# Kernel optimization log

Measured on AMD Instinct MI355X. Metric: run time of the kernel, lower is better.

The kernel has to match this reference:

```python
import jax, jax.numpy as jnp
import numpy as np

# Product-key memory config (matches init_kwargs)
HEADS = 4
K_DIM = 512          # per-head query/key dim; split in two halves of 256
HALF = K_DIM // 2
V_DIM = 512
SUBSIZE = 512        # sub-keys per bank; value table size = SUBSIZE**2
SIZE = SUBSIZE * SUBSIZE
TOPK = 8
TEMP = 1.0
B, T = 4, 2048


def setup_inputs() -> dict:
    key = jax.random.key(0)
    kq, kk, kv = jax.random.split(key, 3)
    bound = 1.0 / np.sqrt(K_DIM)  # reset_parameters: uniform(-1/sqrt(k_dim), 1/sqrt(k_dim))
    query = jax.random.normal(kq, (B, T, HEADS * K_DIM), dtype=jnp.float32)
    keys = jax.random.uniform(kk, (2 * HEADS * SUBSIZE, HALF), dtype=jnp.float32,
                              minval=-bound, maxval=bound)
    # reset_parameters: normal(0, v_dim**-0.5)
    values = jax.random.normal(kv, (SIZE, V_DIM), dtype=jnp.float32) * (V_DIM ** -0.5)
    return {"query": query, "keys": keys, "values": values}


def reference(query, keys, values):
    """retrieve_values: product-key two-stage topk + softmax-weighted embedding bag.
    query: [B, T, HEADS*K_DIM]; keys: [2*HEADS*SUBSIZE, HALF]; values: [SIZE, V_DIM]
    returns retrieved values [B*T, V_DIM].
    """
    Bq, Tq = query.shape[:2]
    N = Bq * Tq
    q = query.reshape(N, HEADS, K_DIM)
    q1, q2 = q[..., :HALF], q[..., HALF:]
    k = keys.reshape(2, HEADS, SUBSIZE, HALF)

    # Sub-key score matmuls (the two 'cdist-like' searches)
    s1 = jnp.einsum('nhd,hsd->nhs', q1, k[0])       # [N, H, SUBSIZE]
    s2 = jnp.einsum('nhd,hsd->nhs', q2, k[1])       # [N, H, SUBSIZE]

    ts1, ti1 = jax.lax.top_k(s1, TOPK)               # [N, H, TOPK]
    ts2, ti2 = jax.lax.top_k(s2, TOPK)

    # Cartesian combination of the two topk sets, then global topk
    comb = (ts1[..., :, None] + ts2[..., None, :]).reshape(N, HEADS, TOPK * TOPK)
    scores, flat_idx = jax.lax.top_k(comb, TOPK)     # [N, H, TOPK]
    sel1 = jnp.take_along_axis(ti1, flat_idx // TOPK, axis=-1)
    sel2 = jnp.take_along_axis(ti2, flat_idx % TOPK, axis=-1)
    indices = sel1 * SUBSIZE + sel2                  # global value-table indices [N, H, TOPK]

    # score_transform: softmax over heads*topk (score_nonlinear='softmax')
    w = jax.nn.softmax(scores.reshape(N, HEADS * TOPK) / TEMP, axis=-1)

    # xformers_embedding_bag: weighted gather-sum over the huge value table
    gathered = values[indices.reshape(N, HEADS * TOPK)]   # [N, H*TOPK, V_DIM]
    vals = jnp.einsum('nk,nkd->nd', w, gathered)          # [N, V_DIM]
    return vals
```

## Files before the change

### kernel.cpp

```cpp
#include <hip/hip_runtime.h>
#include <hip/hip_bf16.h>
#include <math.h>

typedef unsigned short u16;
typedef __attribute__((ext_vector_type(8))) short short8;
typedef __attribute__((ext_vector_type(4))) float f32x4;

#define N_TOK   8192
#define N_HEADS 4
#define KDIM    512
#define HALFD   256
#define VDIM    512
#define SUBK    512
#define NCAND   16

__device__ __forceinline__ u16 f2bf(float f) {
    unsigned u = __float_as_uint(f);
    u += 0x7fffu + ((u >> 16) & 1u);
    return (u16)(u >> 16);
}

__device__ __forceinline__ unsigned med3u(unsigned a, unsigned b, unsigned c) {
    unsigned d;
    asm("v_med3_u32 %0, %1, %2, %3" : "=v"(d) : "v"(a), "v"(b), "v"(c));
    return d;
}

__global__ void k_convert(const float* __restrict__ in, u16* __restrict__ out, int n4) {
    int i = blockIdx.x * blockDim.x + threadIdx.x;
    int stride = gridDim.x * blockDim.x;
    for (; i < n4; i += stride) {
        float4 v = ((const float4*)in)[i];
        unsigned a = (unsigned)f2bf(v.x) | ((unsigned)f2bf(v.y) << 16);
        unsigned b = (unsigned)f2bf(v.z) | ((unsigned)f2bf(v.w) << 16);
        ((uint2*)out)[i] = make_uint2(a, b);
    }
}

__global__ __launch_bounds__(256) void k_score_topk(
    const float* __restrict__ query,
    const u16* __restrict__ kb,
    int* __restrict__ cand)
{
    __shared__ unsigned sc[16 * 513];
    const int nb = blockIdx.x, h = blockIdx.y, half = blockIdx.z;
    const int tid = threadIdx.x;
    const int wave = tid >> 6, l = tid & 63;
    const int lr = l & 15, lk = l >> 4;

    const float* qbase = query + (size_t)(nb * 16 + lr) * (N_HEADS * KDIM)
                       + h * KDIM + half * HALFD + lk * 8;
    short8 a[8];
#pragma unroll
    for (int kf = 0; kf < 8; ++kf) {
        float4 q0 = *(const float4*)(qbase + kf * 32);
        float4 q1 = *(const float4*)(qbase + kf * 32 + 4);
        short8 t;
        t[0] = (short)f2bf(q0.x); t[1] = (short)f2bf(q0.y);
        t[2] = (short)f2bf(q0.z); t[3] = (short)f2bf(q0.w);
        t[4] = (short)f2bf(q1.x); t[5] = (short)f2bf(q1.y);
        t[6] = (short)f2bf(q1.z); t[7] = (short)f2bf(q1.w);
        a[kf] = t;
    }

    const u16* kbase = kb + (size_t)(half * N_HEADS + h) * SUBK * HALFD;
#pragma unroll
    for (int t = 0; t < 8; ++t) {
        const int st = wave * 8 + t;
        const u16* kp = kbase + (size_t)(st * 16 + lr) * HALFD + lk * 8;
        short8 b[8];
#pragma unroll
        for (int kf = 0; kf < 8; ++kf)
            b[kf] = *(const short8*)(kp + kf * 32);
        f32x4 acc = {0.f, 0.f, 0.f, 0.f};
#pragma unroll
        for (int kf = 0; kf < 8; ++kf)
            acc = __builtin_amdgcn_mfma_f32_16x16x32_bf16(a[kf], b[kf], acc, 0, 0, 0);
#pragma unroll
        for (int r = 0; r < 4; ++r) {
            unsigned ub = __float_as_uint(acc[r]);
            unsigned key = ub ^ ((unsigned)((int)ub >> 31) | 0x80000000u);
            key = (key & 0xFFFFFE00u) | (unsigned)(st * 16 + lr);
            sc[(lk * 4 + r) * 513 + st * 16 + lr] = key;
        }
    }
    __syncthreads();

    const int row = tid >> 4, sub = tid & 15;
    unsigned tv[NCAND];
#pragma unroll
    for (int j = 0; j < NCAND; ++j) tv[j] = 0u;
    const int base = row * 513 + sub;
#pragma unroll
    for (int t = 0; t < 32; ++t) {
        unsigned v = sc[base + (t << 4)];
#pragma unroll
        for (int j = NCAND - 1; j >= 1; --j)
            tv[j] = med3u(tv[j - 1], tv[j], v);
        tv[0] = (tv[0] > v) ? tv[0] : v;
    }

    unsigned keep = 0;
#pragma unroll
    for (int r = 0; r < NCAND; ++r) {
        unsigned w = tv[0];
#pragma unroll
        for (int d = 1; d < 16; d <<= 1) {
            unsigned o = __shfl_xor(w, d, 16);
            w = (o > w) ? o : w;
        }
        if (sub == r) keep = w;
        bool pop = (tv[0] == w);
#pragma unroll
        for (int j = 0; j < NCAND - 1; ++j) tv[j] = pop ? tv[j + 1] : tv[j];
        tv[NCAND - 1] = pop ? 0u : tv[NCAND - 1];
    }
    const int n = nb * 16 + row;
    cand[((size_t)n * 8 + (h * 2 + half)) * NCAND + sub] = (int)(keep & 0x1FFu);
}

__global__ __launch_bounds__(256) void k_select_gather(
    const float* __restrict__ query,
    const float* __restrict__ keys,
    const float* __restrict__ values,
    const int* __restrict__ cand,
    float* __restrict__ out)
{
    __shared__ double rv[8][16];
    __shared__ int    ri[8][16];
    __shared__ double tsv[8][8];
    __shared__ int    tsi[8][8];
    __shared__ double s_comb[32];
    __shared__ int    sgi[32];
    __shared__ float  wsm[32];
    __shared__ float  part[4][512];

    const int n = blockIdx.x;
    const int tid = threadIdx.x;

    {
        const int dot = tid >> 1, pt = tid & 1;
        const int g = dot >> 4, j = dot & 15;
        const int h = g >> 1, half = g & 1;
        const int sidx = cand[((size_t)n * 8 + g) * NCAND + j];
        const float* qrow = query + (size_t)n * (N_HEADS * KDIM) + h * KDIM + half * HALFD + pt * 128;
        const float* krow = keys + ((size_t)(half * N_HEADS + h) * SUBK + sidx) * HALFD + pt * 128;
        double a0 = 0, a1 = 0, a2 = 0, a3 = 0;
#pragma unroll 8
        for (int d = 0; d < 128; d += 4) {
            float4 qv = *(const float4*)(qrow + d);
            float4 kv = *(const float4*)(krow + d);
            a0 = fma((double)qv.x, (double)kv.x, a0);
            a1 = fma((double)qv.y, (double)kv.y, a1);
            a2 = fma((double)qv.z, (double)kv.z, a2);
            a3 = fma((double)qv.w, (double)kv.w, a3);
        }
        double s = (a0 + a1) + (a2 + a3);
        double o = __shfl_xor(s, 1);
        if (pt == 0) { rv[g][j] = s + o; ri[g][j] = sidx; }
    }
    __syncthreads();

    if (tid < 128) {
        const int g = tid >> 4, j = tid & 15;
        double v = rv[g][j];
        const int idx = ri[g][j];
        for (int r = 0; r < 8; ++r) {
            double bv = v; int bj = j;
#pragma unroll
            for (int d = 1; d < 16; d <<= 1) {
                double ov = __shfl_xor(bv, d, 16);
                int    oj = __shfl_xor(bj, d, 16);
                if (ov > bv || (ov == bv && oj < bj)) { bv = ov; bj = oj; }
            }
            int widx = __shfl(idx, bj, 16);
            if (j == r) { tsv[g][r] = bv; tsi[g][r] = widx; }
            if (j == bj) v = -1e300;
        }
    }
    __syncthreads();

    {
        const int h = tid >> 6, f = tid & 63;
        double c = tsv[h * 2][f >> 3] + tsv[h * 2 + 1][f & 7];
        for (int r = 0; r < 8; ++r) {
            double bv = c; int bf = f;
#pragma unroll
            for (int d = 1; d < 64; d <<= 1) {
                double ov = __shfl_xor(bv, d, 64);
                int    of = __shfl_xor(bf, d, 64);
                if (ov > bv || (ov == bv && of < bf)) { bv = ov; bf = of; }
            }
            if (f == r) {
                s_comb[h * 8 + r] = bv;
                sgi[h * 8 + r] = tsi[h * 2][bf >> 3] * SUBK + tsi[h * 2 + 1][bf & 7];
            }
            if (f == bf) c = -1e300;
        }
    }
    __syncthreads();

    if (tid < 32) {
        const int k = tid;
        double s = s_comb[k];
        double m = s;
#pragma unroll
        for (int d = 1; d < 32; d <<= 1) m = fmax(m, __shfl_xor(m, d, 32));
        float e = expf((float)(s - m));
        float sum = e;
#pragma unroll
        for (int d = 1; d < 32; d <<= 1) sum += __shfl_xor(sum, d, 32);
        wsm[k] = e / sum;
    }
    __syncthreads();

    {
        const int w = tid >> 6, lane = tid & 63;
        float4 v0[8], v1[8];
#pragma unroll
        for (int r = 0; r < 8; ++r) {
            const float* vr = values + (size_t)sgi[w * 8 + r] * VDIM;
            v0[r] = *(const float4*)(vr + lane * 4);
            v1[r] = *(const float4*)(vr + 256 + lane * 4);
        }
        float4 acc0 = {0.f, 0.f, 0.f, 0.f};
        float4 acc1 = {0.f, 0.f, 0.f, 0.f};
#pragma unroll
        for (int r = 0; r < 8; ++r) {
            const float wk = wsm[w * 8 + r];
            acc0.x = fmaf(wk, v0[r].x, acc0.x);
            acc0.y = fmaf(wk, v0[r].y, acc0.y);
            acc0.z = fmaf(wk, v0[r].z, acc0.z);
            acc0.w = fmaf(wk, v0[r].w, acc0.w);
            acc1.x = fmaf(wk, v1[r].x, acc1.x);
            acc1.y = fmaf(wk, v1[r].y, acc1.y);
            acc1.z = fmaf(wk, v1[r].z, acc1.z);
            acc1.w = fmaf(wk, v1[r].w, acc1.w);
        }
        *(float4*)(&part[w][lane * 4]) = acc0;
        *(float4*)(&part[w][256 + lane * 4]) = acc1;
    }
    __syncthreads();

    {
        const int c = tid * 2;
        float s0 = part[0][c]     + part[1][c]     + part[2][c]     + part[3][c];
        float s1 = part[0][c + 1] + part[1][c + 1] + part[2][c + 1] + part[3][c + 1];
        ((float2*)(out + (size_t)n * VDIM))[tid] = make_float2(s0, s1);
    }
}

extern "C" void kernel_launch(void* const* d_in, const int* in_sizes, int n_in,
                              void* d_out, int out_size, void* d_ws, size_t ws_size,
                              hipStream_t stream) {
    const float* query  = (const float*)d_in[0];
    const float* keys   = (const float*)d_in[1];
    const float* values = (const float*)d_in[2];
    float* out = (float*)d_out;

    char* ws = (char*)d_ws;
    u16* kb   = (u16*)ws;
    int* cand = (int*)(ws + 2097152);

    k_convert<<<512, 256, 0, stream>>>(keys, kb, (2 * N_HEADS * SUBK * HALFD) / 4);

    dim3 gB(N_TOK / 16, N_HEADS, 2);
    k_score_topk<<<gB, 256, 0, stream>>>(query, kb, cand);

    k_select_gather<<<N_TOK, 256, 0, stream>>>(query, keys, values, cand, out);
}
```

Measured before the change: 387.5 us.

## Overlap second-half scoring with first-half select/gather in a mixed kernel

```diff
diff --git a/kernel.cpp b/kernel.cpp
--- a/kernel.cpp
+++ b/kernel.cpp
@@ -37,18 +37,14 @@
     }
 }
 
-__global__ __launch_bounds__(256) void k_score_topk(
-    const float* __restrict__ query,
-    const u16* __restrict__ kb,
-    int* __restrict__ cand)
-{
-    __shared__ unsigned sc[16 * 513];
-    const int nb = blockIdx.x, h = blockIdx.y, half = blockIdx.z;
-    const int tid = threadIdx.x;
+__device__ __forceinline__ void score_body(
+    const float* __restrict__ query, const u16* __restrict__ kb,
+    int* __restrict__ cand, int n0, int h, int half, int tid, unsigned* sc)
+{
     const int wave = tid >> 6, l = tid & 63;
     const int lr = l & 15, lk = l >> 4;
 
-    const float* qbase = query + (size_t)(nb * 16 + lr) * (N_HEADS * KDIM)
+    const float* qbase = query + (size_t)(n0 + lr) * (N_HEADS * KDIM)
                        + h * KDIM + half * HALFD + lk * 8;
     short8 a[8];
 #pragma unroll
@@ -115,28 +111,23 @@
         for (int j = 0; j < NCAND - 1; ++j) tv[j] = pop ? tv[j + 1] : tv[j];
         tv[NCAND - 1] = pop ? 0u : tv[NCAND - 1];
     }
-    const int n = nb * 16 + row;
+    const int n = n0 + row;
     cand[((size_t)n * 8 + (h * 2 + half)) * NCAND + sub] = (int)(keep & 0x1FFu);
 }
 
-__global__ __launch_bounds__(256) void k_select_gather(
-    const float* __restrict__ query,
-    const float* __restrict__ keys,
-    const float* __restrict__ values,
-    const int* __restrict__ cand,
-    float* __restrict__ out)
-{
-    __shared__ double rv[8][16];
-    __shared__ int    ri[8][16];
-    __shared__ double tsv[8][8];
-    __shared__ int    tsi[8][8];
-    __shared__ double s_comb[32];
-    __shared__ int    sgi[32];
-    __shared__ float  wsm[32];
-    __shared__ float  part[4][512];
-
-    const int n = blockIdx.x;
-    const int tid = threadIdx.x;
+__device__ __forceinline__ void sg_body(
+    const float* __restrict__ query, const float* __restrict__ keys,
+    const float* __restrict__ values, const int* __restrict__ cand,
+    float* __restrict__ out, int n, int tid, unsigned char* sm)
+{
+    double* rv     = (double*)(sm);
+    int*    ri     = (int*)(sm + 1024);
+    double* tsv    = (double*)(sm + 1536);
+    int*    tsi    = (int*)(sm + 2048);
+    double* s_comb = (double*)(sm + 2304);
+    int*    sgi    = (int*)(sm + 2560);
+    float*  wsm    = (float*)(sm + 2688);
+    float*  part   = (float*)(sm + 2816);
 
     {
         const int dot = tid >> 1, pt = tid & 1;
@@ -157,14 +148,14 @@
         }
         double s = (a0 + a1) + (a2 + a3);
         double o = __shfl_xor(s, 1);
-        if (pt == 0) { rv[g][j] = s + o; ri[g][j] = sidx; }
+        if (pt == 0) { rv[g * 16 + j] = s + o; ri[g * 16 + j] = sidx; }
     }
     __syncthreads();
 
     if (tid < 128) {
         const int g = tid >> 4, j = tid & 15;
-        double v = rv[g][j];
-        const int idx = ri[g][j];
+        double v = rv[g * 16 + j];
+        const int idx = ri[g * 16 + j];
         for (int r = 0; r < 8; ++r) {
             double bv = v; int bj = j;
 #pragma unroll
@@ -174,7 +165,7 @@
                 if (ov > bv || (ov == bv && oj < bj)) { bv = ov; bj = oj; }
             }
             int widx = __shfl(idx, bj, 16);
-            if (j == r) { tsv[g][r] = bv; tsi[g][r] = widx; }
+            if (j == r) { tsv[g * 8 + r] = bv; tsi[g * 8 + r] = widx; }
             if (j == bj) v = -1e300;
         }
     }
@@ -182,7 +173,7 @@
 
     {
         const int h = tid >> 6, f = tid & 63;
-        double c = tsv[h * 2][f >> 3] + tsv[h * 2 + 1][f & 7];
+        double c = tsv[h * 16 + (f >> 3)] + tsv[(h * 2 + 1) * 8 + (f & 7)];
         for (int r = 0; r < 8; ++r) {
             double bv = c; int bf = f;
 #pragma unroll
@@ -193,7 +184,7 @@
             }
             if (f == r) {
                 s_comb[h * 8 + r] = bv;
-                sgi[h * 8 + r] = tsi[h * 2][bf >> 3] * SUBK + tsi[h * 2 + 1][bf & 7];
+                sgi[h * 8 + r] = tsi[h * 16 + (bf >> 3)] * SUBK + tsi[(h * 2 + 1) * 8 + (bf & 7)];
             }
             if (f == bf) c = -1e300;
         }
@@ -237,17 +228,49 @@
             acc1.z = fmaf(wk, v1[r].z, acc1.z);
             acc1.w = fmaf(wk, v1[r].w, acc1.w);
         }
-        *(float4*)(&part[w][lane * 4]) = acc0;
-        *(float4*)(&part[w][256 + lane * 4]) = acc1;
+        *(float4*)(&part[w * 512 + lane * 4]) = acc0;
+        *(float4*)(&part[w * 512 + 256 + lane * 4]) = acc1;
     }
     __syncthreads();
 
     {
         const int c = tid * 2;
-        float s0 = part[0][c]     + part[1][c]     + part[2][c]     + part[3][c];
-        float s1 = part[0][c + 1] + part[1][c + 1] + part[2][c + 1] + part[3][c + 1];
+        float s0 = part[0 * 512 + c] + part[1 * 512 + c] + part[2 * 512 + c] + part[3 * 512 + c];
+        float s1 = part[0 * 512 + c + 1] + part[1 * 512 + c + 1] + part[2 * 512 + c + 1] + part[3 * 512 + c + 1];
         ((float2*)(out + (size_t)n * VDIM))[tid] = make_float2(s0, s1);
     }
+}
+
+__global__ __launch_bounds__(256) void k_score(
+    const float* __restrict__ query, const u16* __restrict__ kb, int* __restrict__ cand)
+{
+    __shared__ unsigned sc[16 * 513];
+    score_body(query, kb, cand, blockIdx.x * 16, blockIdx.y, blockIdx.z, threadIdx.x, sc);
+}
+
+__global__ __launch_bounds__(256) void k_mixed(
+    const float* __restrict__ query, const u16* __restrict__ kb,
+    const float* __restrict__ keys, const float* __restrict__ values,
+    int* __restrict__ cand, float* __restrict__ out)
+{
+    __shared__ __align__(16) unsigned char smem[16 * 513 * 4];
+    const int i = blockIdx.x;
+    const int q = i / 3, m = i - q * 3;
+    if (m == 0) {
+        const int nb = q & 255, h = (q >> 8) & 3, half = q >> 10;
+        score_body(query, kb, cand, 4096 + nb * 16, h, half, threadIdx.x, (unsigned*)smem);
+    } else {
+        sg_body(query, keys, values, cand, out, 2 * q + (m - 1), threadIdx.x, smem);
+    }
+}
+
+__global__ __launch_bounds__(256) void k_sg(
+    const float* __restrict__ query, const float* __restrict__ keys,
+    const float* __restrict__ values, const int* __restrict__ cand,
+    float* __restrict__ out)
+{
+    __shared__ __align__(16) unsigned char smem[11008];
+    sg_body(query, keys, values, cand, out, 4096 + blockIdx.x, threadIdx.x, smem);
 }
 
 extern "C" void kernel_launch(void* const* d_in, const int* in_sizes, int n_in,
@@ -264,8 +287,10 @@
 
     k_convert<<<512, 256, 0, stream>>>(keys, kb, (2 * N_HEADS * SUBK * HALFD) / 4);
 
-    dim3 gB(N_TOK / 16, N_HEADS, 2);
-    k_score_topk<<<gB, 256, 0, stream>>>(query, kb, cand);
-
-    k_select_gather<<<N_TOK, 256, 0, stream>>>(query, keys, values, cand, out);
-}
+    dim3 gA(256, N_HEADS, 2);
+    k_score<<<gA, 256, 0, stream>>>(query, kb, cand);
+
+    k_mixed<<<6144, 256, 0, stream>>>(query, kb, keys, values, cand, out);
+
+    k_sg<<<4096, 256, 0, stream>>>(query, keys, values, cand, out);
+}
```

Measured after the change: 404.9 us. 1.04x slower.
